# Kernel tuning notes

Measured on AMD Instinct MI355X. Metric: run time of the kernel, lower is better.

## Reference

```python
import jax, jax.numpy as jnp
import numpy as np

IMG_SIZE = 32
PATCH_SIZE = 4
GRID = IMG_SIZE // PATCH_SIZE  # 8 -> 64 patches
EMBED = 768
PATCH_DIM = 1 * 3 * PATCH_SIZE * PATCH_SIZE  # 48
BATCH = 1024


def setup_inputs() -> dict:
    key = jax.random.key(0)
    k1, k2, k3, k4 = jax.random.split(key, 4)
    x = jax.random.normal(k1, (BATCH, 1, 3, IMG_SIZE, IMG_SIZE), dtype=jnp.float32)
    W = jax.random.normal(k2, (EMBED, PATCH_DIM), dtype=jnp.float32) * 0.02  # fc1.weight [out,in]
    cls_token = jax.random.normal(k3, (1, EMBED), dtype=jnp.float32)
    pos_emb = jax.random.normal(k4, (1, GRID * GRID + 1, EMBED), dtype=jnp.float32)
    return {"x": x, "W": W, "cls_token": cls_token, "pos_emb": pos_emb}


def reference(x, W, cls_token, pos_emb):
    B, D1, C, H, Wd = x.shape
    # Row-major patch extraction matching the loop (col fast, row slow).
    # patch flatten order = (D1, C, ph, pw), identical to nn.Flatten(1) on [B,D1,C,P,P].
    patches = x.reshape(B, D1, C, GRID, PATCH_SIZE, GRID, PATCH_SIZE)
    patches = patches.transpose(0, 3, 5, 1, 2, 4, 6)  # [B, gr, gc, D1, C, P, P]
    patches = patches.reshape(B, GRID * GRID, D1 * C * PATCH_SIZE * PATCH_SIZE)  # [B,64,48]
    proj = jnp.einsum('bnp,ep->bne', patches, W)  # fc1 (no bias) -> [B,64,E]
    cls = jnp.broadcast_to(cls_token[None, :, :], (B, 1, EMBED))
    s = jnp.concatenate([cls, proj], axis=1)  # [B,65,E]
    return pos_emb + s
```

## Files before the change

### kernel.cpp

```cpp
#include <hip/hip_runtime.h>


#define BATCH   1024
#define EMBED   768
#define NPATCH  64
#define SEQ     65
#define OUTB    (SEQ * EMBED)
#define WELEMS  (EMBED * 48)

typedef __attribute__((ext_vector_type(8))) short bf16x8;
typedef __attribute__((ext_vector_type(4))) float f32x4;

__device__ __forceinline__ short f2bf(float f) {
    union { float f; unsigned u; } v; v.f = f;
    unsigned r = v.u + 0x7FFFu + ((v.u >> 16) & 1u);
    return (short)(r >> 16);
}

__global__ __launch_bounds__(256) void prep_kernel(const float* __restrict__ W,
                                                   const float* __restrict__ cls,
                                                   const float* __restrict__ pos,
                                                   short* __restrict__ w16,
                                                   float* __restrict__ out) {
    const int tid = threadIdx.x;
    const int bid = blockIdx.x;
    if (bid < 18) {
        const int i = (bid * 256 + tid) * 8;
        float4 u0 = *(const float4*)(W + i);
        float4 u1 = *(const float4*)(W + i + 4);
        bf16x8 v;
        v[0] = f2bf(u0.x); v[1] = f2bf(u0.y); v[2] = f2bf(u0.z); v[3] = f2bf(u0.w);
        v[4] = f2bf(u1.x); v[5] = f2bf(u1.y); v[6] = f2bf(u1.z); v[7] = f2bf(u1.w);
        *(bf16x8*)(w16 + i) = v;
    } else {
        const int b = bid - 18;
        if (tid < 192) {
            f32x4 cv = ((const f32x4*)cls)[tid];
            f32x4 pv = ((const f32x4*)pos)[tid];
            ((f32x4*)out)[(size_t)b * (OUTB / 4) + tid] = cv + pv;
        }
    }
}

__global__ __launch_bounds__(256, 4) void patch_embed_main(const float* __restrict__ x,
                                                           const short* __restrict__ w16,
                                                           const float* __restrict__ pos,
                                                           float* __restrict__ out) {
    __shared__ short A[16 * 64];

    const int tid  = threadIdx.x;
    const int lane = tid & 63;
    const int wave = tid >> 6;
    const int lr   = lane & 15;
    const int lg   = lane >> 4;
    const int bid  = blockIdx.x;
    const int b    = bid >> 3;
    const int sub  = bid & 7;
    const int mt   = sub >> 1;
    const int eh   = sub & 1;
    const int ebase = eh * 384 + wave * 96;

    if (tid < 128) {
        const int row = tid >> 3;
        const int kb  = tid & 7;
        short* dst = &A[row * 64 + ((kb ^ (row & 7)) * 8)];
        bf16x8 v = {0, 0, 0, 0, 0, 0, 0, 0};
        if (kb < 6) {
            const int n   = mt * 16 + row;
            const int c   = kb >> 1;
            const int ph0 = (kb & 1) * 2;
            const int gr = n >> 3, gc = n & 7;
            const float* src = x + (size_t)b * 3072 + c * 1024 + (gr * 4 + ph0) * 32 + gc * 4;
            float4 u0 = *(const float4*)src;
            float4 u1 = *(const float4*)(src + 32);
            v[0] = f2bf(u0.x); v[1] = f2bf(u0.y); v[2] = f2bf(u0.z); v[3] = f2bf(u0.w);
            v[4] = f2bf(u1.x); v[5] = f2bf(u1.y); v[6] = f2bf(u1.z); v[7] = f2bf(u1.w);
        }
        *(bf16x8*)dst = v;
    }

    bf16x8 bw[6][2];
    #pragma unroll
    for (int nt = 0; nt < 6; ++nt) {
        const short* wrow = w16 + (ebase + nt * 16 + lr) * 48;
        bw[nt][0] = *(const bf16x8*)(wrow + lg * 8);
        const int k1 = 32 + lg * 8;
        bf16x8 f = {0, 0, 0, 0, 0, 0, 0, 0};
        if (k1 < 48) f = *(const bf16x8*)(wrow + k1);
        bw[nt][1] = f;
    }

    __syncthreads();

    bf16x8 a0 = *(const bf16x8*)&A[lr * 64 + ((lg ^ (lr & 7)) * 8)];
    bf16x8 a1 = *(const bf16x8*)&A[lr * 64 + (((4 + lg) ^ (lr & 7)) * 8)];

    f32x4 acc[6];
    const f32x4 zero = {0.f, 0.f, 0.f, 0.f};
    #pragma unroll
    for (int nt = 0; nt < 6; ++nt)
        acc[nt] = __builtin_amdgcn_mfma_f32_16x16x32_bf16(a0, bw[nt][0], zero, 0, 0, 0);
    #pragma unroll
    for (int nt = 0; nt < 6; ++nt)
        acc[nt] = __builtin_amdgcn_mfma_f32_16x16x32_bf16(a1, bw[nt][1], acc[nt], 0, 0, 0);

    #pragma unroll
    for (int j = 0; j < 4; ++j) {
        const int n = mt * 16 + lg * 4 + j;
        const float* prow = pos + (size_t)(n + 1) * EMBED + ebase + lr;
        float* orow = out + (size_t)b * OUTB + (size_t)(n + 1) * EMBED + ebase + lr;
        #pragma unroll
        for (int nt = 0; nt < 6; ++nt)
            orow[nt * 16] = acc[nt][j] + prow[nt * 16];
    }
}

extern "C" void kernel_launch(void* const* d_in, const int* in_sizes, int n_in,
                              void* d_out, int out_size, void* d_ws, size_t ws_size,
                              hipStream_t stream) {
    const float* x   = (const float*)d_in[0];
    const float* W   = (const float*)d_in[1];
    const float* cls = (const float*)d_in[2];
    const float* pos = (const float*)d_in[3];
    float* out = (float*)d_out;
    short* w16 = (short*)d_ws;

    hipLaunchKernelGGL(prep_kernel, dim3(18 + BATCH), dim3(256), 0, stream,
                       W, cls, pos, w16, out);
    hipLaunchKernelGGL(patch_embed_main, dim3(BATCH * 8), dim3(256), 0, stream,
                       x, w16, pos, out);
}
```

Baseline: 47.69 us.

## Process all 64 patches per block to reuse weight fragments across M tiles

Each block now handles a whole image half (all four 16-row M tiles) instead of a single M tile, which cuts the grid from 8192 to 2048 blocks. The bf16 weight fragments loaded into registers are reused four times, and the whole image patch matrix is staged in LDS once. Positional-embedding loads are issued before the MFMAs in each iteration so they can overlap with the matrix math. The trade-off is fewer blocks to hide latency, a serial loop over M tiles, and higher register and LDS use per block.

```diff
diff --git a/kernel.cpp b/kernel.cpp
--- a/kernel.cpp
+++ b/kernel.cpp
@@ -46,7 +46,7 @@
                                                            const short* __restrict__ w16,
                                                            const float* __restrict__ pos,
                                                            float* __restrict__ out) {
-    __shared__ short A[16 * 64];
+    __shared__ short A[64 * 64];
 
     const int tid  = threadIdx.x;
     const int lane = tid & 63;
@@ -54,22 +54,21 @@
     const int lr   = lane & 15;
     const int lg   = lane >> 4;
     const int bid  = blockIdx.x;
-    const int b    = bid >> 3;
-    const int sub  = bid & 7;
-    const int mt   = sub >> 1;
-    const int eh   = sub & 1;
+    const int b    = bid >> 1;
+    const int eh   = bid & 1;
     const int ebase = eh * 384 + wave * 96;
 
-    if (tid < 128) {
-        const int row = tid >> 3;
-        const int kb  = tid & 7;
+    #pragma unroll
+    for (int i = 0; i < 2; ++i) {
+        const int cid = tid + i * 256;
+        const int row = cid >> 3;
+        const int kb  = cid & 7;
         short* dst = &A[row * 64 + ((kb ^ (row & 7)) * 8)];
         bf16x8 v = {0, 0, 0, 0, 0, 0, 0, 0};
         if (kb < 6) {
-            const int n   = mt * 16 + row;
             const int c   = kb >> 1;
             const int ph0 = (kb & 1) * 2;
-            const int gr = n >> 3, gc = n & 7;
+            const int gr = row >> 3, gc = row & 7;
             const float* src = x + (size_t)b * 3072 + c * 1024 + (gr * 4 + ph0) * 32 + gc * 4;
             float4 u0 = *(const float4*)src;
             float4 u1 = *(const float4*)(src + 32);
@@ -92,26 +91,39 @@
 
     __syncthreads();
 
-    bf16x8 a0 = *(const bf16x8*)&A[lr * 64 + ((lg ^ (lr & 7)) * 8)];
-    bf16x8 a1 = *(const bf16x8*)&A[lr * 64 + (((4 + lg) ^ (lr & 7)) * 8)];
+    const size_t outb = (size_t)b * OUTB + EMBED;
+    const f32x4 zero = {0.f, 0.f, 0.f, 0.f};
+    #pragma unroll 1
+    for (int mt = 0; mt < 4; ++mt) {
+        float pv[4][6];
+        #pragma unroll
+        for (int j = 0; j < 4; ++j) {
+            const int n = mt * 16 + lg * 4 + j;
+            const float* pr = pos + (size_t)(n + 1) * EMBED + ebase + lr;
+            #pragma unroll
+            for (int nt = 0; nt < 6; ++nt) pv[j][nt] = pr[nt * 16];
+        }
 
-    f32x4 acc[6];
-    const f32x4 zero = {0.f, 0.f, 0.f, 0.f};
-    #pragma unroll
-    for (int nt = 0; nt < 6; ++nt)
-        acc[nt] = __builtin_amdgcn_mfma_f32_16x16x32_bf16(a0, bw[nt][0], zero, 0, 0, 0);
-    #pragma unroll
-    for (int nt = 0; nt < 6; ++nt)
-        acc[nt] = __builtin_amdgcn_mfma_f32_16x16x32_bf16(a1, bw[nt][1], acc[nt], 0, 0, 0);
+        const int arow = mt * 16 + lr;
+        bf16x8 a0 = *(const bf16x8*)&A[arow * 64 + ((lg ^ (arow & 7)) * 8)];
+        bf16x8 a1 = *(const bf16x8*)&A[arow * 64 + (((4 + lg) ^ (arow & 7)) * 8)];
 
-    #pragma unroll
-    for (int j = 0; j < 4; ++j) {
-        const int n = mt * 16 + lg * 4 + j;
-        const float* prow = pos + (size_t)(n + 1) * EMBED + ebase + lr;
-        float* orow = out + (size_t)b * OUTB + (size_t)(n + 1) * EMBED + ebase + lr;
+        f32x4 acc[6];
         #pragma unroll
         for (int nt = 0; nt < 6; ++nt)
-            orow[nt * 16] = acc[nt][j] + prow[nt * 16];
+            acc[nt] = __builtin_amdgcn_mfma_f32_16x16x32_bf16(a0, bw[nt][0], zero, 0, 0, 0);
+        #pragma unroll
+        for (int nt = 0; nt < 6; ++nt)
+            acc[nt] = __builtin_amdgcn_mfma_f32_16x16x32_bf16(a1, bw[nt][1], acc[nt], 0, 0, 0);
+
+        #pragma unroll
+        for (int j = 0; j < 4; ++j) {
+            const int n = mt * 16 + lg * 4 + j;
+            float* orow = out + outb + (size_t)n * EMBED + ebase + lr;
+            #pragma unroll
+            for (int nt = 0; nt < 6; ++nt)
+                orow[nt * 16] = acc[nt][j] + pv[j][nt];
+        }
     }
 }
 
@@ -127,6 +139,6 @@
 
     hipLaunchKernelGGL(prep_kernel, dim3(18 + BATCH), dim3(256), 0, stream,
                        W, cls, pos, w16, out);
-    hipLaunchKernelGGL(patch_embed_main, dim3(BATCH * 8), dim3(256), 0, stream,
+    hipLaunchKernelGGL(patch_embed_main, dim3(BATCH * 2), dim3(256), 0, stream,
                        x, w16, pos, out);
 }
```

Measured after the change: 46.22 us. -3.1%, faster.
